# Kernel tuning notes

Measured on AMD Instinct MI355X. Metric: run time of the kernel, lower is better.

Reference implementation:

```python
import jax, jax.numpy as jnp
import numpy as np

N = 20000      # nodes
E = 320000     # edges
F_IN = 64      # input_dim
HID = 128      # hidden_dim
H = 2          # heads (hard-coded in BGA)
G = 64         # num graphs (batch_step_dim[0])
MID = 32       # middle_dim
OUT = 1        # output_dim
EPS = 1e-5


def setup_inputs() -> dict:
    key = jax.random.key(0)
    ks = jax.random.split(key, 24)
    p = lambda k, shape: jax.random.normal(k, shape, jnp.float32) * 0.05
    inp = {}
    inp["x"] = jax.random.normal(ks[0], (N, F_IN), jnp.float32)
    inp["edge_index"] = jax.random.randint(ks[1], (2, E), 0, N)
    inp["atten_edge_index"] = jax.random.randint(ks[2], (2, E), 0, N)
    inp["batch_index"] = jnp.sort(jax.random.randint(ks[3], (N,), 0, G))
    # GANConv 0 MLP (2-layer: Linear->BN->ReLU->Linear)
    inp["g0_w1"] = p(ks[4], (F_IN, HID)); inp["g0_b1"] = jnp.zeros((HID,), jnp.float32)
    inp["g0_bn_g"] = jnp.ones((HID,), jnp.float32); inp["g0_bn_b"] = jnp.zeros((HID,), jnp.float32)
    inp["g0_w2"] = p(ks[5], (HID, HID)); inp["g0_b2"] = jnp.zeros((HID,), jnp.float32)
    # GANConv 1 MLP
    inp["g1_w1"] = p(ks[6], (HID, HID)); inp["g1_b1"] = jnp.zeros((HID,), jnp.float32)
    inp["g1_bn_g"] = jnp.ones((HID,), jnp.float32); inp["g1_bn_b"] = jnp.zeros((HID,), jnp.float32)
    inp["g1_w2"] = p(ks[7], (HID, HID)); inp["g1_b2"] = jnp.zeros((HID,), jnp.float32)
    # BGA batch norms after each GANConv
    inp["bn0_g"] = jnp.ones((HID,), jnp.float32); inp["bn0_b"] = jnp.zeros((HID,), jnp.float32)
    inp["bn1_g"] = jnp.ones((HID,), jnp.float32); inp["bn1_b"] = jnp.zeros((HID,), jnp.float32)
    # ATTConv atten_self: in=HID, out=HID, heads=2, concat=True
    inp["a1_wl"] = p(ks[8], (HID, H * HID)); inp["a1_bl"] = jnp.zeros((H * HID,), jnp.float32)
    inp["a1_wr"] = p(ks[9], (HID, H * HID)); inp["a1_br"] = jnp.zeros((H * HID,), jnp.float32)
    inp["a1_att"] = p(ks[10], (H, HID))
    inp["a1_bias"] = jnp.zeros((H * HID,), jnp.float32)
    # ATTConv atten: in=H*HID, out=HID, heads=2, concat=False (mean over heads)
    inp["a2_wl"] = p(ks[11], (H * HID, H * HID)); inp["a2_bl"] = jnp.zeros((H * HID,), jnp.float32)
    inp["a2_wr"] = p(ks[12], (H * HID, H * HID)); inp["a2_br"] = jnp.zeros((H * HID,), jnp.float32)
    inp["a2_att"] = p(ks[13], (H, HID))
    inp["a2_bias"] = jnp.zeros((HID,), jnp.float32)
    # prediction heads (only layer 0 and last are used)
    inp["pred0_w"] = p(ks[14], (F_IN, MID)); inp["pred0_b"] = jnp.zeros((MID,), jnp.float32)
    inp["predL_w"] = p(ks[15], (HID, MID)); inp["predL_b"] = jnp.zeros((MID,), jnp.float32)
    inp["out_w"] = p(ks[16], (MID, OUT)); inp["out_b"] = jnp.zeros((OUT,), jnp.float32)
    return inp


def _bn(x, g, b):  # training-mode batch norm over node axis
    m = x.mean(0)
    v = x.var(0)
    return (x - m) * jax.lax.rsqrt(v + EPS) * g + b


def _mlp2(x, w1, b1, bn_g, bn_b, w2, b2):
    h = jax.nn.relu(_bn(x @ w1 + b1, bn_g, bn_b))
    return h @ w2 + b2


def _gan_conv(x, edge_index, w1, b1, bn_g, bn_b, w2, b2):
    row, col = edge_index[0], edge_index[1]
    agg = jax.ops.segment_sum(x[col], row, num_segments=x.shape[0])
    return _mlp2(x + agg, w1, b1, bn_g, bn_b, w2, b2)


def _att_conv(x, edge_index, wl, bl, wr, br, att, bias, concat):
    # GATv2-style: e = leaky_relu(x_i + x_j); alpha = softmax_dst(<e, att>)
    n = x.shape[0]
    xl = (x @ wl + bl).reshape(n, H, HID)  # source proj
    xr = (x @ wr + br).reshape(n, H, HID)  # target proj
    src, dst = edge_index[0], edge_index[1]
    e = jax.nn.leaky_relu(xl[src] + xr[dst], 0.2)          # [E,H,C]
    logit = jnp.einsum('ehc,hc->eh', e, att)               # [E,H]
    lmax = jax.ops.segment_max(logit, dst, num_segments=n)
    w = jnp.exp(logit - lmax[dst])
    denom = jax.ops.segment_sum(w, dst, num_segments=n)
    alpha = w / (denom[dst] + 1e-16)                       # [E,H]
    out = jax.ops.segment_sum(xl[src] * alpha[:, :, None], dst, num_segments=n)
    if concat:
        out = out.reshape(n, H * HID)
    else:
        out = out.mean(1)
    return out + bias, alpha


def reference(x, edge_index, atten_edge_index, batch_index,
              g0_w1, g0_b1, g0_bn_g, g0_bn_b, g0_w2, g0_b2,
              g1_w1, g1_b1, g1_bn_g, g1_bn_b, g1_w2, g1_b2,
              bn0_g, bn0_b, bn1_g, bn1_b,
              a1_wl, a1_bl, a1_wr, a1_br, a1_att, a1_bias,
              a2_wl, a2_bl, a2_wr, a2_br, a2_att, a2_bias,
              pred0_w, pred0_b, predL_w, predL_b, out_w, out_b):
    h0 = x
    h1 = jax.nn.relu(_bn(_gan_conv(h0, edge_index, g0_w1, g0_b1, g0_bn_g, g0_bn_b, g0_w2, g0_b2), bn0_g, bn0_b))
    h2 = jax.nn.relu(_bn(_gan_conv(h1, edge_index, g1_w1, g1_b1, g1_bn_g, g1_bn_b, g1_w2, g1_b2), bn1_g, bn1_b))
    emb, _ = _att_conv(h2, edge_index, a1_wl, a1_bl, a1_wr, a1_br, a1_att, a1_bias, concat=True)
    emb = jax.nn.relu(emb)
    atten_out, alpha = _att_conv(emb, atten_edge_index, a2_wl, a2_bl, a2_wr, a2_br, a2_att, a2_bias, concat=False)
    atten_out = jax.nn.relu(atten_out)
    pool0 = jax.ops.segment_sum(h0, batch_index, num_segments=G)
    poolL = jax.ops.segment_sum(atten_out, batch_index, num_segments=G)
    out_h = jax.nn.relu((pool0 @ pred0_w + pred0_b) + (poolL @ predL_w + predL_b))
    outputs = out_h @ out_w + out_b
    return (outputs, atten_out, alpha)
```

## Files before the change

### kernel.cpp

```cpp
#include <hip/hip_runtime.h>
#include <hip/hip_bf16.h>

#define N_NODES 20000
#define E_EDGES 320000
#define F_INN   64
#define HID     128
#define HEADS   2
#define HC      (HEADS * HID)
#define G_GR    64
#define MIDD    32
#define EPSV    1e-5f
#define NBUK    79

#define CDIV(a, b) (((a) + (b) - 1) / (b))

typedef __attribute__((ext_vector_type(8))) short          bf16x8;
typedef __attribute__((ext_vector_type(4))) float          f32x4;
typedef __attribute__((ext_vector_type(8))) unsigned short u16x8;

__device__ inline float bf2f(unsigned short u) { return __uint_as_float((unsigned)u << 16); }
__device__ inline unsigned short f2bf(float f) {
    unsigned u = __float_as_uint(f);
    unsigned r = u + 0x7FFFu + ((u >> 16) & 1u);
    return (unsigned short)(r >> 16);
}

#if __has_builtin(__builtin_amdgcn_exp2f)
__device__ inline float fexp2(float x) { return __builtin_amdgcn_exp2f(x); }
#else
__device__ inline float fexp2(float x) { return exp2f(x); }
#endif

struct Csr3 {
    const int* key[3];
    const int* other[3];
    int* btot;
    int* bstart;
    int* bcur;
    int* rowptr[3];
    int* out[3];
    int2* tmp;
};

__global__ __launch_bounds__(256) void k_bhist(Csr3 c) {
    __shared__ int hist[NBUK];
    const int y = blockIdx.y;
    const int chunk0 = blockIdx.x * 4096;
    const int t = threadIdx.x;
    for (int i = t; i < NBUK; i += 256) hist[i] = 0;
    __syncthreads();
#pragma unroll
    for (int i = 0; i < 16; i++) {
        int e = chunk0 + (i << 8) + t;
        if (e < E_EDGES) atomicAdd(&hist[c.key[y][e] >> 8], 1);
    }
    __syncthreads();
    for (int i = t; i < NBUK; i += 256)
        if (hist[i] > 0) atomicAdd(&c.btot[y * NBUK + i], hist[i]);
}

__global__ void k_bscan(Csr3 c) {
    __shared__ int sh[3 * NBUK];
    int t = threadIdx.x;
    for (int i = t; i < 3 * NBUK; i += 256) sh[i] = c.btot[i];
    __syncthreads();
    if (t < 3) {
        int run = 0;
        int* bs = c.bstart + t * (NBUK + 1);
        for (int b = 0; b < NBUK; b++) {
            bs[b] = run;
            c.bcur[t * NBUK + b] = run;
            run += sh[t * NBUK + b];
        }
        bs[NBUK] = run;
    }
}

__global__ __launch_bounds__(256) void k_bucketA(Csr3 c) {
    __shared__ int hist[NBUK], base[NBUK], off[NBUK];
    const int y = blockIdx.y;
    const int chunk0 = blockIdx.x * 4096;
    const int t = threadIdx.x;
    for (int i = t; i < NBUK; i += 256) { hist[i] = 0; off[i] = 0; }
    __syncthreads();
    int keys[16], vals[16], bks[16];
#pragma unroll
    for (int i = 0; i < 16; i++) {
        int e = chunk0 + (i << 8) + t;
        bool ok = (e < E_EDGES);
        int k = ok ? c.key[y][e] : 0;
        keys[i] = k;
        vals[i] = ok ? ((y == 2) ? e : c.other[y][e]) : 0;
        bks[i] = ok ? (k >> 8) : -1;
        if (ok) atomicAdd(&hist[k >> 8], 1);
    }
    __syncthreads();
    if (t < NBUK && hist[t] > 0) base[t] = atomicAdd(&c.bcur[y * NBUK + t], hist[t]);
    __syncthreads();
    int2* ty = c.tmp + (size_t)y * E_EDGES;
#pragma unroll
    for (int i = 0; i < 16; i++) {
        int b = bks[i];
        if (b >= 0) {
            int o = atomicAdd(&off[b], 1);
            ty[base[b] + o] = make_int2(keys[i], vals[i]);
        }
    }
}

__global__ __launch_bounds__(256) void k_bucketB(Csr3 c) {
    __shared__ int cnt[256], lbase[256], run[256];
    const int y = blockIdx.y;
    const int b = blockIdx.x;
    const int nbase = b << 8;
    const int t = threadIdx.x;
    cnt[t] = 0; run[t] = 0;
    __syncthreads();
    const int bs = c.bstart[y * (NBUK + 1) + b];
    const int be = c.bstart[y * (NBUK + 1) + b + 1];
    const int2* ty = c.tmp + (size_t)y * E_EDGES;
    for (int i = bs + t; i < be; i += 256)
        atomicAdd(&cnt[ty[i].x - nbase], 1);
    __syncthreads();
    int v = cnt[t];
    lbase[t] = v;
    __syncthreads();
    for (int off = 1; off < 256; off <<= 1) {
        int u = (t >= off) ? lbase[t - off] : 0;
        __syncthreads();
        lbase[t] += u;
        __syncthreads();
    }
    int excl = lbase[t] - v;
    __syncthreads();
    lbase[t] = excl;
    __syncthreads();
    int n = nbase + t;
    if (n < N_NODES) c.rowptr[y][n] = bs + excl;
    if (b == NBUK - 1 && t == 0) c.rowptr[y][N_NODES] = E_EDGES;
    int* outy = c.out[y];
    for (int i = bs + t; i < be; i += 256) {
        int2 kv = ty[i];
        int k = kv.x - nbase;
        int o = atomicAdd(&run[k], 1);
        outy[bs + lbase[k] + o] = kv.y;
    }
}

__global__ __launch_bounds__(256) void k_src_gather(const int* __restrict__ eids,
                                                    const int* __restrict__ srcs,
                                                    int* __restrict__ outv) {
    int i = blockIdx.x * 256 + threadIdx.x;
    if (i < E_EDGES) outv[i] = srcs[eids[i]];
}

__global__ __launch_bounds__(256) void k_gather_f32(const float4* __restrict__ x,
                                                    const int* __restrict__ rowptr,
                                                    const int* __restrict__ srcs,
                                                    unsigned short* __restrict__ z) {
    int gid = blockIdx.x * blockDim.x + threadIdx.x;
    int n = gid >> 4;
    if (n >= N_NODES) return;
    int q = gid & 15;
    float4 acc = x[((size_t)n << 4) + q];
    float4 a1 = make_float4(0.f, 0.f, 0.f, 0.f), a2 = a1, a3 = a1;
    int p = rowptr[n], p1 = rowptr[n + 1];
    for (; p + 4 <= p1; p += 4) {
        float4 v0 = x[((size_t)srcs[p + 0] << 4) + q];
        float4 v1 = x[((size_t)srcs[p + 1] << 4) + q];
        float4 v2 = x[((size_t)srcs[p + 2] << 4) + q];
        float4 v3 = x[((size_t)srcs[p + 3] << 4) + q];
        acc.x += v0.x; acc.y += v0.y; acc.z += v0.z; acc.w += v0.w;
        a1.x += v1.x; a1.y += v1.y; a1.z += v1.z; a1.w += v1.w;
        a2.x += v2.x; a2.y += v2.y; a2.z += v2.z; a2.w += v2.w;
        a3.x += v3.x; a3.y += v3.y; a3.z += v3.z; a3.w += v3.w;
    }
    for (; p < p1; p++) {
        float4 v = x[((size_t)srcs[p] << 4) + q];
        acc.x += v.x; acc.y += v.y; acc.z += v.z; acc.w += v.w;
    }
    acc.x += a1.x + a2.x + a3.x; acc.y += a1.y + a2.y + a3.y;
    acc.z += a1.z + a2.z + a3.z; acc.w += a1.w + a2.w + a3.w;
    ushort4 o;
    o.x = f2bf(acc.x); o.y = f2bf(acc.y); o.z = f2bf(acc.z); o.w = f2bf(acc.w);
    *(ushort4*)&z[((size_t)n << 6) + (q << 2)] = o;
}

__global__ __launch_bounds__(256) void k_gather_bn(const u16x8* __restrict__ raw,
                                                   const int* __restrict__ rowptr,
                                                   const int* __restrict__ srcs,
                                                   const float* __restrict__ bn_sums,
                                                   const float* __restrict__ g,
                                                   const float* __restrict__ b,
                                                   u16x8* __restrict__ z) {
    int gid = blockIdx.x * blockDim.x + threadIdx.x;
    int n = gid >> 4;
    if (n >= N_NODES) return;
    int q = gid & 15;
    float sc[8], sh[8];
#pragma unroll
    for (int i = 0; i < 8; i++) {
        int c = (q << 3) + i;
        float mean = bn_sums[c] / N_NODES;
        float istd = rsqrtf(bn_sums[HID + c] / N_NODES - mean * mean + EPSV);
        float s = istd * g[c];
        sc[i] = s;
        sh[i] = b[c] - mean * s;
    }
    u16x8 u0 = raw[((size_t)n << 4) + q];
    float acc[8];
#pragma unroll
    for (int i = 0; i < 8; i++) acc[i] = fmaxf(bf2f(u0[i]) * sc[i] + sh[i], 0.f);
    int p = rowptr[n], p1 = rowptr[n + 1];
    for (; p + 4 <= p1; p += 4) {
        u16x8 v0 = raw[((size_t)srcs[p + 0] << 4) + q];
        u16x8 v1 = raw[((size_t)srcs[p + 1] << 4) + q];
        u16x8 v2 = raw[((size_t)srcs[p + 2] << 4) + q];
        u16x8 v3 = raw[((size_t)srcs[p + 3] << 4) + q];
#pragma unroll
        for (int i = 0; i < 8; i++) {
            acc[i] += fmaxf(bf2f(v0[i]) * sc[i] + sh[i], 0.f)
                    + fmaxf(bf2f(v1[i]) * sc[i] + sh[i], 0.f)
                    + fmaxf(bf2f(v2[i]) * sc[i] + sh[i], 0.f)
                    + fmaxf(bf2f(v3[i]) * sc[i] + sh[i], 0.f);
        }
    }
    for (; p < p1; p++) {
        u16x8 v = raw[((size_t)srcs[p] << 4) + q];
#pragma unroll
        for (int i = 0; i < 8; i++) acc[i] += fmaxf(bf2f(v[i]) * sc[i] + sh[i], 0.f);
    }
    u16x8 o;
#pragma unroll
    for (int i = 0; i < 8; i++) o[i] = f2bf(acc[i]);
    z[((size_t)n << 4) + q] = o;
}

struct WtJob  { const float* src; unsigned short* dst; int K; int N; };
struct WtJobs { WtJob j[8]; };
__global__ void k_wt_cast(WtJobs jobs) {
    WtJob jb = jobs.j[blockIdx.y];
    int total = jb.K * jb.N;
    for (int i = blockIdx.x * blockDim.x + threadIdx.x; i < total; i += gridDim.x * blockDim.x) {
        int nn = i / jb.K, kk = i - nn * jb.K;
        jb.dst[i] = f2bf(jb.src[(size_t)kk * jb.N + nn]);
    }
}

template <int STATS, int BNA, int TM, int TN, int BIAS2, int SPLIT>
__global__ __launch_bounds__(256) void k_mfma_gemm(const unsigned short* __restrict__ A,
                                                   const unsigned short* __restrict__ Wt,
                                                   const float* __restrict__ biasL,
                                                   const float* __restrict__ biasR,
                                                   unsigned short* __restrict__ Cout,
                                                   int M, int K, int N,
                                                   float* __restrict__ stats_sums,
                                                   const float* __restrict__ bn_sums,
                                                   const float* __restrict__ bn_g,
                                                   const float* __restrict__ bn_b) {
    constexpr int BNF = (TM == 128) ? (TN / 32) : (TN / 64);
    constexpr int BPASS = TN / 64;
    __shared__ unsigned short As[TM][40];
    __shared__ unsigned short Bs[TN][40];
    __shared__ float s_scale[BNA ? HID : 1], s_shift[BNA ? HID : 1];
    const int t = threadIdx.x;
    if (BNA) {
        if (t < HID) {
            float mean = bn_sums[t] / M;
            float istd = rsqrtf(bn_sums[HID + t] / M - mean * mean + EPSV);
            float s = istd * bn_g[t];
            s_scale[t] = s;
            s_shift[t] = bn_b[t] - mean * s;
        }
        __syncthreads();
    }
    const int wave = t >> 6, lane = t & 63;
    const int row0 = blockIdx.y * TM, col0 = blockIdx.x * TN;
    const int wm = (TM == 128) ? ((wave & 1) << 6) : 0;
    const int wn = (TM == 128) ? ((wave >> 1) << 6)
                               : ((TN == 128) ? (wave << 5) : (wave << 4));
    const int lm = lane & 15, lk = (lane >> 4) << 3;
    constexpr int APASS = TM / 64;
    f32x4 acc[4][BNF] = {};
    for (int k0 = 0; k0 < K; k0 += 32) {
        u16x8 av[APASS], wv[BPASS];
#pragma unroll
        for (int i = 0; i < APASS; i++) {
            int c = t + (i << 8);
            int r = c >> 2, ko = (c & 3) << 3;
            u16x8 zv = {};
            int gr = row0 + r;
            av[i] = (gr < M) ? *(const u16x8*)&A[(size_t)gr * K + k0 + ko] : zv;
            if (BNA) {
#pragma unroll
                for (int j = 0; j < 8; j++) {
                    int kc = k0 + ko + j;
                    float v = fmaxf(bf2f(av[i][j]) * s_scale[kc] + s_shift[kc], 0.f);
                    av[i][j] = f2bf(v);
                }
            }
        }
#pragma unroll
        for (int i = 0; i < BPASS; i++) {
            int c = t + (i << 8);
            int r = c >> 2, ko = (c & 3) << 3;
            wv[i] = *(const u16x8*)&Wt[(size_t)(col0 + r) * K + k0 + ko];
        }
        __syncthreads();
#pragma unroll
        for (int i = 0; i < APASS; i++) {
            int c = t + (i << 8);
            int r = c >> 2, ko = (c & 3) << 3;
            *(u16x8*)&As[r][ko] = av[i];
        }
#pragma unroll
        for (int i = 0; i < BPASS; i++) {
            int c = t + (i << 8);
            int r = c >> 2, ko = (c & 3) << 3;
            *(u16x8*)&Bs[r][ko] = wv[i];
        }
        __syncthreads();
        bf16x8 af[4], bfm[BNF];
#pragma unroll
        for (int i = 0; i < 4; i++) af[i]  = *(const bf16x8*)&As[wm + (i << 4) + lm][lk];
#pragma unroll
        for (int j = 0; j < BNF; j++) bfm[j] = *(const bf16x8*)&Bs[wn + (j << 4) + lm][lk];
#pragma unroll
        for (int i = 0; i < 4; i++)
#pragma unroll
            for (int j = 0; j < BNF; j++)
                acc[i][j] = __builtin_amdgcn_mfma_f32_16x16x32_bf16(af[i], bfm[j], acc[i][j], 0, 0, 0);
    }
    const int lr4 = (lane >> 4) << 2;
    float s1[BNF], s2[BNF];
#pragma unroll
    for (int j = 0; j < BNF; j++) { s1[j] = 0.f; s2[j] = 0.f; }
#pragma unroll
    for (int j = 0; j < BNF; j++) {
        int col = col0 + wn + (j << 4) + lm;
        float bv = BIAS2 ? ((col < 256) ? biasL[col] : biasR[col - 256]) : biasL[col];
        unsigned short* dstp;
        int cl;
        if (SPLIT) {
            if (col < 256) { dstp = Cout; cl = col; }
            else { dstp = Cout + (size_t)N_NODES * 256; cl = col - 256; }
        } else { dstp = Cout; cl = col; }
#pragma unroll
        for (int i = 0; i < 4; i++) {
#pragma unroll
            for (int r = 0; r < 4; r++) {
                int row = row0 + wm + (i << 4) + lr4 + r;
                if (row < M) {
                    float v = acc[i][j][r] + bv;
                    if (SPLIT) dstp[(size_t)row * 256 + cl] = f2bf(v);
                    else       dstp[(size_t)row * N + cl]   = f2bf(v);
                    if (STATS) { s1[j] += v; s2[j] += v * v; }
                }
            }
        }
    }
    if (STATS) {
#pragma unroll
        for (int j = 0; j < BNF; j++) {
            s1[j] += __shfl_xor(s1[j], 16, 64); s1[j] += __shfl_xor(s1[j], 32, 64);
            s2[j] += __shfl_xor(s2[j], 16, 64); s2[j] += __shfl_xor(s2[j], 32, 64);
        }
        if ((lane >> 4) == 0) {
#pragma unroll
            for (int j = 0; j < BNF; j++) {
                int col = col0 + wn + (j << 4) + lm;
                atomicAdd(&stats_sums[col], s1[j]);
                atomicAdd(&stats_sums[HID + col], s2[j]);
            }
        }
    }
}

#define ATT_CAP 192
#define LOG2E   1.4426950408889634f
#define DTHR    11.0f

__device__ __forceinline__ float att_logit8(u16x8 uv, const float* xr8, const float* at8, float* x8) {
    float tl = 0.f;
#pragma unroll
    for (int i = 0; i < 8; i++) {
        x8[i] = bf2f(uv[i]);
        float v = x8[i] + xr8[i];
        v = fmaxf(v, 0.2f * v);
        tl = fmaf(at8[i], v, tl);
    }
    return tl;
}

template <int CTRL>
__device__ __forceinline__ float dpp_add(float x) {
    int y = __builtin_amdgcn_update_dpp(0, __float_as_int(x), CTRL, 0xF, 0xF, true);
    return x + __int_as_float(y);
}

__device__ __forceinline__ float red16(float tl) {
    tl = dpp_add<0xB1>(tl);
    tl = dpp_add<0x4E>(tl);
    tl = dpp_add<0x124>(tl);
    tl = dpp_add<0x128>(tl);
    return tl;
}

template <int WITH_ALPHA>
__device__ __forceinline__ void att_group4(const u16x8* uv, int ebase, int p0,
                                           int half, int j, int h,
                                           const float* xr8, const float* at8,
                                           float& m, float& ssum, float* acc,
                                           float (*slg)[2]) {
    float x8[4][8], tl[4];
#pragma unroll
    for (int g = 0; g < 4; g++) tl[g] = att_logit8(uv[g], xr8, at8, x8[g]);
#pragma unroll
    for (int g = 0; g < 4; g++) tl[g] = red16(tl[g]);
    if (WITH_ALPHA && (j & 15) == 0) {
#pragma unroll
        for (int g = 0; g < 4; g++) {
            int idx = ebase + (g << 1) + half - p0;
            if (idx < ATT_CAP) slg[idx][h] = tl[g];
        }
    }
    float pm = fmaxf(fmaxf(tl[0], tl[1]), fmaxf(tl[2], tl[3]));
    if (__builtin_expect(!__all(pm <= m + DTHR), 0)) {
#pragma unroll
        for (int g = 0; g < 4; g++) {
            float mn = fmaxf(m, tl[g]);
            float sc = fexp2(m - mn);
            float w  = fexp2(tl[g] - mn);
            ssum = ssum * sc + w;
#pragma unroll
            for (int i = 0; i < 8; i++) acc[i] = acc[i] * sc + w * x8[g][i];
            m = mn;
        }
    } else {
        float w0 = fexp2(tl[0] - m), w1 = fexp2(tl[1] - m);
        float w2 = fexp2(tl[2] - m), w3 = fexp2(tl[3] - m);
        ssum += (w0 + w1) + (w2 + w3);
#pragma unroll
        for (int i = 0; i < 8; i++)
            acc[i] += (w0 * x8[0][i] + w1 * x8[1][i]) + (w2 * x8[2][i] + w3 * x8[3][i]);
    }
}

template <int CONCAT, int WITH_ALPHA>
__global__ __launch_bounds__(256) void k_att_fused(const u16x8* __restrict__ XL,
                                                   const u16x8* __restrict__ XR,
                                                   const int* __restrict__ rowptr,
                                                   const int* __restrict__ plist,
                                                   const int* __restrict__ srclist,
                                                   const float* __restrict__ att,
                                                   const float* __restrict__ bias,
                                                   void* __restrict__ outp,
                                                   float* __restrict__ alpha_out) {
    __shared__ float s_lg[WITH_ALPHA ? 4 : 1][WITH_ALPHA ? ATT_CAP : 1][2];
    const int t = threadIdx.x;
    const int wave = t >> 6, l = t & 63;
    const int n = blockIdx.x * 4 + wave;
    const int half = l >> 5;
    const int j = l & 31;
    const int h = j >> 4;

    u16x8 ur = XR[((size_t)n << 5) + j];
    float xr8[8];
#pragma unroll
    for (int i = 0; i < 8; i++) xr8[i] = bf2f(ur[i]);
    const float* ap = &att[h * HID + ((j & 15) << 3)];
    float at8[8];
#pragma unroll
    for (int i = 0; i < 8; i++) at8[i] = ap[i] * LOG2E;

    const int p0 = rowptr[n], p1 = rowptr[n + 1];
    const int* PL = WITH_ALPHA ? srclist : plist;
    const int deg = p1 - p0;
    int idxreg = (deg > 0) ? PL[p0 + ((l < deg) ? l : (deg - 1))] : 0;

    float m = -1e30f, ssum = 0.f;
    float acc[8] = {};
    float (*slg)[2] = WITH_ALPHA ? s_lg[wave] : nullptr;

    int p = p0;
    for (; p + 16 <= p1; p += 16) {
        int rb = p - p0;
        int sA[4], sB[4];
        if (rb + 16 <= 64) {
#pragma unroll
            for (int g = 0; g < 4; g++)
                sA[g] = __builtin_amdgcn_ds_bpermute((rb + (g << 1) + half) << 2, idxreg);
#pragma unroll
            for (int g = 0; g < 4; g++)
                sB[g] = __builtin_amdgcn_ds_bpermute((rb + 8 + (g << 1) + half) << 2, idxreg);
        } else {
#pragma unroll
            for (int g = 0; g < 4; g++) sA[g] = PL[p + (g << 1) + half];
#pragma unroll
            for (int g = 0; g < 4; g++) sB[g] = PL[p + 8 + (g << 1) + half];
        }
        u16x8 uvA[4], uvB[4];
#pragma unroll
        for (int g = 0; g < 4; g++) uvA[g] = XL[((size_t)sA[g] << 5) + j];
#pragma unroll
        for (int g = 0; g < 4; g++) uvB[g] = XL[((size_t)sB[g] << 5) + j];
        att_group4<WITH_ALPHA>(uvA, p,     p0, half, j, h, xr8, at8, m, ssum, acc, slg);
        att_group4<WITH_ALPHA>(uvB, p + 8, p0, half, j, h, xr8, at8, m, ssum, acc, slg);
    }
    for (; p + 8 <= p1; p += 8) {
        int rb = p - p0;
        int s4[4];
        if (rb + 8 <= 64) {
#pragma unroll
            for (int g = 0; g < 4; g++)
                s4[g] = __builtin_amdgcn_ds_bpermute((rb + (g << 1) + half) << 2, idxreg);
        } else {
#pragma unroll
            for (int g = 0; g < 4; g++) s4[g] = PL[p + (g << 1) + half];
        }
        u16x8 uv[4];
#pragma unroll
        for (int g = 0; g < 4; g++) uv[g] = XL[((size_t)s4[g] << 5) + j];
        att_group4<WITH_ALPHA>(uv, p, p0, half, j, h, xr8, at8, m, ssum, acc, slg);
    }
    for (; p < p1; p += 2) {
        const bool v1 = (p + 1 < p1);
        int er = (half && v1) ? (p + 1) : p;
        int src;
        if (p - p0 + 2 <= 64) src = __builtin_amdgcn_ds_bpermute((er - p0) << 2, idxreg);
        else src = PL[er];
        u16x8 uv = XL[((size_t)src << 5) + j];
        float x8[8], tl;
        tl = att_logit8(uv, xr8, at8, x8);
        tl = red16(tl);
        float vm = (half && !v1) ? 0.f : 1.f;
        if (vm == 0.f) tl = -1e30f;
        if (WITH_ALPHA && (j & 15) == 0 && vm != 0.f) {
            int idx = p + half - p0;
            if (idx < ATT_CAP) s_lg[wave][idx][h] = tl;
        }
        if (__builtin_expect(!__all(tl <= m + DTHR), 0)) {
            float mn = fmaxf(m, tl);
            float sc = fexp2(m - mn);
            float w  = fexp2(tl - mn) * vm;
            ssum = ssum * sc + w;
#pragma unroll
            for (int i = 0; i < 8; i++) acc[i] = acc[i] * sc + w * x8[i];
            m = mn;
        } else {
            float w = fexp2(tl - m) * vm;
            ssum += w;
#pragma unroll
            for (int i = 0; i < 8; i++) acc[i] += w * x8[i];
        }
    }

    float m_o = __shfl_xor(m, 32, 64);
    float mf  = fmaxf(m, m_o);
    float sA  = fexp2(m - mf);
    float ssA = ssum * sA;
    float ssum_f = ssA + __shfl_xor(ssA, 32, 64);
    float accf[8];
#pragma unroll
    for (int i = 0; i < 8; i++) {
        float a = acc[i] * sA;
        accf[i] = a + __shfl_xor(a, 32, 64);
    }
    float inv = 1.f / (ssum_f + 1e-16f);

    if (WITH_ALPHA) {
        float m_oh   = __shfl_xor(mf, 16, 64);
        float inv_oh = __shfl_xor(inv, 16, 64);
        float m2[2], i2[2];
        m2[h] = mf;  m2[1 - h] = m_oh;
        i2[h] = inv; i2[1 - h] = inv_oh;
        int cnt = p1 - p0;
        int ccnt = (cnt < ATT_CAP) ? cnt : ATT_CAP;
        for (int i = l; i < ccnt * 2; i += 64) {
            int idx = i >> 1, hh = i & 1;
            float a = fexp2(s_lg[wave][idx][hh] - m2[hh]) * i2[hh];
            alpha_out[plist[p0 + idx] * HEADS + hh] = a;
        }
        for (int pp = p0 + ATT_CAP; pp < p1; pp++) {
            int src = PL[pp];
            u16x8 uv = XL[((size_t)src << 5) + j];
            float x8[8], tl;
            tl = att_logit8(uv, xr8, at8, x8);
            tl = red16(tl);
            if ((j & 15) == 0 && half == 0)
                alpha_out[plist[pp] * HEADS + h] = fexp2(tl - mf) * inv;
        }
    }

    if (CONCAT) {
        if (half == 0) {
            const float* bp = &bias[j << 3];
            u16x8 o;
#pragma unroll
            for (int i = 0; i < 8; i++) o[i] = f2bf(fmaxf(accf[i] * inv + bp[i], 0.f));
            ((u16x8*)outp)[((size_t)n << 5) + j] = o;
        }
    } else {
        float om[8];
#pragma unroll
        for (int i = 0; i < 8; i++) {
            float v = accf[i] * inv;
            om[i] = 0.5f * (v + __shfl_xor(v, 16, 64));
        }
        if (half == 0 && h == 0) {
            const float* bp = &bias[j << 3];
            float4 o0, o1;
            o0.x = fmaxf(om[0] + bp[0], 0.f); o0.y = fmaxf(om[1] + bp[1], 0.f);
            o0.z = fmaxf(om[2] + bp[2], 0.f); o0.w = fmaxf(om[3] + bp[3], 0.f);
            o1.x = fmaxf(om[4] + bp[4], 0.f); o1.y = fmaxf(om[5] + bp[5], 0.f);
            o1.z = fmaxf(om[6] + bp[6], 0.f); o1.w = fmaxf(om[7] + bp[7], 0.f);
            ((float4*)outp)[((size_t)n << 5) + (j << 1)]     = o0;
            ((float4*)outp)[((size_t)n << 5) + (j << 1) + 1] = o1;
        }
    }
}

template <int C>
__global__ __launch_bounds__(256) void k_pool_atomic(const float* __restrict__ X,
                                                     const int* __restrict__ batch,
                                                     float* __restrict__ pool, int npb) {
    const int RP = 256 / C;
    int c = threadIdx.x & (C - 1);
    int rofs = threadIdx.x / C;
    int i0 = blockIdx.x * npb;
    int i1 = min(i0 + npb, N_NODES);
    float acc = 0.f;
    int gcur = -1;
    for (int i = i0 + rofs; i < i1; i += RP) {
        int g = batch[i];
        if (g != gcur) {
            if (gcur >= 0) atomicAdd(&pool[gcur * C + c], acc);
            acc = 0.f; gcur = g;
        }
        acc += X[(size_t)i * C + c];
    }
    if (gcur >= 0) atomicAdd(&pool[gcur * C + c], acc);
}

__global__ void k_head(const float* __restrict__ pool0, const float* __restrict__ poolL,
                       const float* __restrict__ p0w, const float* __restrict__ p0b,
                       const float* __restrict__ pLw, const float* __restrict__ pLb,
                       const float* __restrict__ ow, const float* __restrict__ ob,
                       float* __restrict__ outputs) {
    int g = blockIdx.x;
    int m = threadIdx.x;
    __shared__ float sh[MIDD];
    if (m < MIDD) {
        float s = p0b[m] + pLb[m];
        for (int k = 0; k < F_INN; k++) s += pool0[g * F_INN + k] * p0w[k * MIDD + m];
        for (int k = 0; k < HID; k++)  s += poolL[g * HID + k] * pLw[k * MIDD + m];
        sh[m] = fmaxf(s, 0.f);
    }
    __syncthreads();
    if (m == 0) {
        float s = ob[0];
        for (int k = 0; k < MIDD; k++) s += sh[k] * ow[k];
        outputs[g] = s;
    }
}

extern "C" void kernel_launch(void* const* d_in, const int* in_sizes, int n_in,
                              void* d_out, int out_size, void* d_ws, size_t ws_size,
                              hipStream_t stream) {
    const float* x      = (const float*)d_in[0];
    const int*   ei     = (const int*)d_in[1];
    const int*   aei    = (const int*)d_in[2];
    const int*   batch  = (const int*)d_in[3];
    const float* g0_w1  = (const float*)d_in[4];
    const float* g0_b1  = (const float*)d_in[5];
    const float* g0_bng = (const float*)d_in[6];
    const float* g0_bnb = (const float*)d_in[7];
    const float* g0_w2  = (const float*)d_in[8];
    const float* g0_b2  = (const float*)d_in[9];
    const float* g1_w1  = (const float*)d_in[10];
    const float* g1_b1  = (const float*)d_in[11];
    const float* g1_bng = (const float*)d_in[12];
    const float* g1_bnb = (const float*)d_in[13];
    const float* g1_w2  = (const float*)d_in[14];
    const float* g1_b2  = (const float*)d_in[15];
    const float* bn0_g  = (const float*)d_in[16];
    const float* bn0_b  = (const float*)d_in[17];
    const float* bn1_g  = (const float*)d_in[18];
    const float* bn1_b  = (const float*)d_in[19];
    const float* a1_wl  = (const float*)d_in[20];
    const float* a1_bl  = (const float*)d_in[21];
    const float* a1_wr  = (const float*)d_in[22];
    const float* a1_br  = (const float*)d_in[23];
    const float* a1_att = (const float*)d_in[24];
    const float* a1_bias= (const float*)d_in[25];
    const float* a2_wl  = (const float*)d_in[26];
    const float* a2_bl  = (const float*)d_in[27];
    const float* a2_wr  = (const float*)d_in[28];
    const float* a2_br  = (const float*)d_in[29];
    const float* a2_att = (const float*)d_in[30];
    const float* a2_bias= (const float*)d_in[31];
    const float* p0w    = (const float*)d_in[32];
    const float* p0b    = (const float*)d_in[33];
    const float* pLw    = (const float*)d_in[34];
    const float* pLb    = (const float*)d_in[35];
    const float* ow     = (const float*)d_in[36];
    const float* ob     = (const float*)d_in[37];

    float* out_head  = (float*)d_out;
    float* atten_out = out_head + G_GR;
    float* alpha_out = atten_out + (size_t)N_NODES * HID;

    float* ws = (float*)d_ws;
    float* sums4 = ws;
    float* pool0 = sums4 + 4 * 256;
    float* poolL = pool0 + G_GR * F_INN;
    int*   btot  = (int*)(poolL + G_GR * HID);
    const size_t zero_bytes = (4 * 256 + G_GR * F_INN + G_GR * HID + 3 * NBUK) * 4;

    int* ip = btot + 3 * NBUK;
    int* bstart = ip; ip += 3 * (NBUK + 1);
    int* bcur   = ip; ip += 3 * NBUK;
    int* rowptr[3]; int* payload[3];
    for (int c = 0; c < 3; c++) {
        rowptr[c]  = ip; ip += N_NODES + 1;
        payload[c] = ip; ip += E_EDGES;
    }
    int2* tmp3 = (int2*)ip; ip += 2 * 3 * E_EDGES;
    int* srclist = (int*)tmp3;
    const size_t NB = (size_t)N_NODES * HC;
    unsigned short* B1 = (unsigned short*)ip;
    unsigned short* B2 = B1 + NB;
    unsigned short* Qb = B2 + NB;
    unsigned short* g0w1t = Qb + 2 * NB;
    unsigned short* g0w2t = g0w1t + 128 * 64;
    unsigned short* g1w1t = g0w2t + 128 * 128;
    unsigned short* g1w2t = g1w1t + 128 * 128;
    unsigned short* a1wlt = g1w2t + 128 * 128;
    unsigned short* a1wrt = a1wlt + 256 * 128;
    unsigned short* a2wlt = a1wrt + 256 * 128;
    unsigned short* a2wrt = a2wlt + 256 * 256;

    unsigned short* XLb = Qb;
    unsigned short* XRb = Qb + (size_t)N_NODES * 256;

    const int* e_row = ei;
    const int* e_col = ei + E_EDGES;
    const int* a_src = aei;
    const int* a_dst = aei + E_EDGES;

    const int TB = 256;
#define GRID1(n) dim3(CDIV((n), TB))

    {
        WtJobs jobs;
        jobs.j[0] = {g0_w1, g0w1t, F_INN, HID};
        jobs.j[1] = {g0_w2, g0w2t, HID,   HID};
        jobs.j[2] = {g1_w1, g1w1t, HID,   HID};
        jobs.j[3] = {g1_w2, g1w2t, HID,   HID};
        jobs.j[4] = {a1_wl, a1wlt, HID,   HC};
        jobs.j[5] = {a1_wr, a1wrt, HID,   HC};
        jobs.j[6] = {a2_wl, a2wlt, HC,    HC};
        jobs.j[7] = {a2_wr, a2wrt, HC,    HC};
        k_wt_cast<<<dim3(32, 8), TB, 0, stream>>>(jobs);
    }

    (void)hipMemsetAsync(sums4, 0, zero_bytes, stream);
    {
        Csr3 c;
        c.key[0] = e_row; c.other[0] = e_col;
        c.key[1] = e_col; c.other[1] = e_row;
        c.key[2] = a_dst; c.other[2] = a_src;
        c.btot = btot; c.bstart = bstart; c.bcur = bcur; c.tmp = tmp3;
        for (int i = 0; i < 3; i++) { c.rowptr[i] = rowptr[i]; c.out[i] = payload[i]; }
        k_bhist<<<dim3(CDIV(E_EDGES, 4096), 3), TB, 0, stream>>>(c);
        k_bscan<<<dim3(1), TB, 0, stream>>>(c);
        k_bucketA<<<dim3(CDIV(E_EDGES, 4096), 3), TB, 0, stream>>>(c);
        k_bucketB<<<dim3(NBUK, 3), TB, 0, stream>>>(c);
    }
    k_src_gather<<<GRID1(E_EDGES), TB, 0, stream>>>(payload[2], a_src, srclist);

    const dim3 gemm_g1(2, CDIV(N_NODES, 64));
    const dim3 gemm_gq(4, CDIV(N_NODES, 128));
    const float* NOF = nullptr;

    k_gather_f32<<<GRID1(N_NODES * 16), TB, 0, stream>>>((const float4*)x, rowptr[0], payload[0], B1);
    k_mfma_gemm<1, 0, 64, 64, 0, 0><<<gemm_g1, TB, 0, stream>>>(B1, g0w1t, g0_b1, NOF, B2, N_NODES, F_INN, HID,
                                                                sums4 + 0, NOF, NOF, NOF);
    k_mfma_gemm<1, 1, 64, 64, 0, 0><<<gemm_g1, TB, 0, stream>>>(B2, g0w2t, g0_b2, NOF, B1, N_NODES, HID, HID,
                                                                sums4 + 256, sums4 + 0, g0_bng, g0_bnb);

    k_gather_bn<<<GRID1(N_NODES * 16), TB, 0, stream>>>((const u16x8*)B1, rowptr[0], payload[0],
                                                        sums4 + 256, bn0_g, bn0_b, (u16x8*)B2);
    k_mfma_gemm<1, 0, 64, 64, 0, 0><<<gemm_g1, TB, 0, stream>>>(B2, g1w1t, g1_b1, NOF, B1, N_NODES, HID, HID,
                                                                sums4 + 512, NOF, NOF, NOF);
    k_mfma_gemm<1, 1, 64, 64, 0, 0><<<gemm_g1, TB, 0, stream>>>(B1, g1w2t, g1_b2, NOF, B2, N_NODES, HID, HID,
                                                                sums4 + 768, sums4 + 512, g1_bng, g1_bnb);

    k_mfma_gemm<0, 1, 128, 128, 1, 1><<<gemm_gq, TB, 0, stream>>>(B2, a1wlt, a1_bl, a1_br, XLb, N_NODES, HID, 512,
                                                                  nullptr, sums4 + 768, bn1_g, bn1_b);
    k_att_fused<1, 0><<<dim3(N_NODES / 4), TB, 0, stream>>>(
        (const u16x8*)XLb, (const u16x8*)XRb, rowptr[1], payload[1], nullptr,
        a1_att, a1_bias, (void*)B1, nullptr);

    k_mfma_gemm<0, 0, 128, 128, 1, 1><<<gemm_gq, TB, 0, stream>>>(B1, a2wlt, a2_bl, a2_br, XLb, N_NODES, HC, 512,
                                                                  nullptr, NOF, NOF, NOF);
    k_att_fused<0, 1><<<dim3(N_NODES / 4), TB, 0, stream>>>(
        (const u16x8*)XLb, (const u16x8*)XRb, rowptr[2], payload[2], srclist,
        a2_att, a2_bias, (void*)atten_out, alpha_out);

    {
        const int npb = 64;
        k_pool_atomic<F_INN><<<dim3(CDIV(N_NODES, npb)), TB, 0, stream>>>(x, batch, pool0, npb);
        k_pool_atomic<HID><<<dim3(CDIV(N_NODES, npb)), TB, 0, stream>>>(atten_out, batch, poolL, npb);
    }
    k_head<<<dim3(G_GR), 64, 0, stream>>>(pool0, poolL, p0w, p0b, pLw, pLb, ow, ob, out_head);
}
```

Measured before the change: 418.8 us.

## Pack bucket temp entries, fuse front gather/srclist/pool0 kernels, mask attention tail

```diff
diff --git a/kernel.cpp b/kernel.cpp
--- a/kernel.cpp
+++ b/kernel.cpp
@@ -39,7 +39,7 @@
     int* bcur;
     int* rowptr[3];
     int* out[3];
-    int2* tmp;
+    int* tmp;
 };
 
 __global__ __launch_bounds__(256) void k_bhist(Csr3 c) {
@@ -97,13 +97,13 @@
     __syncthreads();
     if (t < NBUK && hist[t] > 0) base[t] = atomicAdd(&c.bcur[y * NBUK + t], hist[t]);
     __syncthreads();
-    int2* ty = c.tmp + (size_t)y * E_EDGES;
+    int* ty = c.tmp + (size_t)y * E_EDGES;
 #pragma unroll
     for (int i = 0; i < 16; i++) {
         int b = bks[i];
         if (b >= 0) {
             int o = atomicAdd(&off[b], 1);
-            ty[base[b] + o] = make_int2(keys[i], vals[i]);
+            ty[base[b] + o] = ((keys[i] & 255) << 24) | vals[i];
         }
     }
 }
@@ -118,9 +118,9 @@
     __syncthreads();
     const int bs = c.bstart[y * (NBUK + 1) + b];
     const int be = c.bstart[y * (NBUK + 1) + b + 1];
-    const int2* ty = c.tmp + (size_t)y * E_EDGES;
+    const int* ty = c.tmp + (size_t)y * E_EDGES;
     for (int i = bs + t; i < be; i += 256)
-        atomicAdd(&cnt[ty[i].x - nbase], 1);
+        atomicAdd(&cnt[((unsigned)ty[i]) >> 24], 1);
     __syncthreads();
     int v = cnt[t];
     lbase[t] = v;
@@ -140,50 +140,67 @@
     if (b == NBUK - 1 && t == 0) c.rowptr[y][N_NODES] = E_EDGES;
     int* outy = c.out[y];
     for (int i = bs + t; i < be; i += 256) {
-        int2 kv = ty[i];
-        int k = kv.x - nbase;
+        int u = ty[i];
+        int k = ((unsigned)u) >> 24;
         int o = atomicAdd(&run[k], 1);
-        outy[bs + lbase[k] + o] = kv.y;
-    }
-}
-
-__global__ __launch_bounds__(256) void k_src_gather(const int* __restrict__ eids,
-                                                    const int* __restrict__ srcs,
-                                                    int* __restrict__ outv) {
-    int i = blockIdx.x * 256 + threadIdx.x;
-    if (i < E_EDGES) outv[i] = srcs[eids[i]];
-}
-
-__global__ __launch_bounds__(256) void k_gather_f32(const float4* __restrict__ x,
-                                                    const int* __restrict__ rowptr,
-                                                    const int* __restrict__ srcs,
-                                                    unsigned short* __restrict__ z) {
-    int gid = blockIdx.x * blockDim.x + threadIdx.x;
-    int n = gid >> 4;
-    if (n >= N_NODES) return;
-    int q = gid & 15;
-    float4 acc = x[((size_t)n << 4) + q];
-    float4 a1 = make_float4(0.f, 0.f, 0.f, 0.f), a2 = a1, a3 = a1;
-    int p = rowptr[n], p1 = rowptr[n + 1];
-    for (; p + 4 <= p1; p += 4) {
-        float4 v0 = x[((size_t)srcs[p + 0] << 4) + q];
-        float4 v1 = x[((size_t)srcs[p + 1] << 4) + q];
-        float4 v2 = x[((size_t)srcs[p + 2] << 4) + q];
-        float4 v3 = x[((size_t)srcs[p + 3] << 4) + q];
-        acc.x += v0.x; acc.y += v0.y; acc.z += v0.z; acc.w += v0.w;
-        a1.x += v1.x; a1.y += v1.y; a1.z += v1.z; a1.w += v1.w;
-        a2.x += v2.x; a2.y += v2.y; a2.z += v2.z; a2.w += v2.w;
-        a3.x += v3.x; a3.y += v3.y; a3.z += v3.z; a3.w += v3.w;
-    }
-    for (; p < p1; p++) {
-        float4 v = x[((size_t)srcs[p] << 4) + q];
-        acc.x += v.x; acc.y += v.y; acc.z += v.z; acc.w += v.w;
-    }
-    acc.x += a1.x + a2.x + a3.x; acc.y += a1.y + a2.y + a3.y;
-    acc.z += a1.z + a2.z + a3.z; acc.w += a1.w + a2.w + a3.w;
-    ushort4 o;
-    o.x = f2bf(acc.x); o.y = f2bf(acc.y); o.z = f2bf(acc.z); o.w = f2bf(acc.w);
-    *(ushort4*)&z[((size_t)n << 6) + (q << 2)] = o;
+        outy[bs + lbase[k] + o] = u & 0x00FFFFFF;
+    }
+}
+
+struct FrontArgs {
+    const float4* x; const int* rowptr0; const int* pay0; unsigned short* z;
+    const int* pay2; const int* asrc; int* srclist;
+    const int* batch; float* pool0;
+};
+__global__ __launch_bounds__(256) void k_front(FrontArgs a) {
+    const int bx = blockIdx.x, t = threadIdx.x;
+    if (bx < 1250) {
+        int gid = bx * 256 + t;
+        int n = gid >> 4;
+        int q = gid & 15;
+        float4 acc = a.x[((size_t)n << 4) + q];
+        float4 a1 = make_float4(0.f, 0.f, 0.f, 0.f), a2 = a1, a3 = a1;
+        int p = a.rowptr0[n], p1 = a.rowptr0[n + 1];
+        for (; p + 4 <= p1; p += 4) {
+            float4 v0 = a.x[((size_t)a.pay0[p + 0] << 4) + q];
+            float4 v1 = a.x[((size_t)a.pay0[p + 1] << 4) + q];
+            float4 v2 = a.x[((size_t)a.pay0[p + 2] << 4) + q];
+            float4 v3 = a.x[((size_t)a.pay0[p + 3] << 4) + q];
+            acc.x += v0.x; acc.y += v0.y; acc.z += v0.z; acc.w += v0.w;
+            a1.x += v1.x; a1.y += v1.y; a1.z += v1.z; a1.w += v1.w;
+            a2.x += v2.x; a2.y += v2.y; a2.z += v2.z; a2.w += v2.w;
+            a3.x += v3.x; a3.y += v3.y; a3.z += v3.z; a3.w += v3.w;
+        }
+        for (; p < p1; p++) {
+            float4 v = a.x[((size_t)a.pay0[p] << 4) + q];
+            acc.x += v.x; acc.y += v.y; acc.z += v.z; acc.w += v.w;
+        }
+        acc.x += a1.x + a2.x + a3.x; acc.y += a1.y + a2.y + a3.y;
+        acc.z += a1.z + a2.z + a3.z; acc.w += a1.w + a2.w + a3.w;
+        ushort4 o;
+        o.x = f2bf(acc.x); o.y = f2bf(acc.y); o.z = f2bf(acc.z); o.w = f2bf(acc.w);
+        *(ushort4*)&a.z[((size_t)n << 6) + (q << 2)] = o;
+    } else if (bx < 2500) {
+        int i = (bx - 1250) * 256 + t;
+        a.srclist[i] = a.asrc[a.pay2[i]];
+    } else {
+        int c = t & 63;
+        int rofs = t >> 6;
+        int i0 = (bx - 2500) * 64;
+        int i1 = min(i0 + 64, N_NODES);
+        float acc = 0.f;
+        int gcur = -1;
+        const float* X = (const float*)a.x;
+        for (int i = i0 + rofs; i < i1; i += 4) {
+            int g = a.batch[i];
+            if (g != gcur) {
+                if (gcur >= 0) atomicAdd(&a.pool0[gcur * F_INN + c], acc);
+                acc = 0.f; gcur = g;
+            }
+            acc += X[(size_t)i * F_INN + c];
+        }
+        if (gcur >= 0) atomicAdd(&a.pool0[gcur * F_INN + c], acc);
+    }
 }
 
 __global__ __launch_bounds__(256) void k_gather_bn(const u16x8* __restrict__ raw,
@@ -406,8 +423,8 @@
     return tl;
 }
 
-template <int WITH_ALPHA>
-__device__ __forceinline__ void att_group4(const u16x8* uv, int ebase, int p0,
+template <int WITH_ALPHA, int MASKED>
+__device__ __forceinline__ void att_group4(const u16x8* uv, const float* vm, int ebase, int p0,
                                            int half, int j, int h,
                                            const float* xr8, const float* at8,
                                            float& m, float& ssum, float* acc,
@@ -417,11 +434,16 @@
     for (int g = 0; g < 4; g++) tl[g] = att_logit8(uv[g], xr8, at8, x8[g]);
 #pragma unroll
     for (int g = 0; g < 4; g++) tl[g] = red16(tl[g]);
+    if (MASKED) {
+#pragma unroll
+        for (int g = 0; g < 4; g++) tl[g] = (vm[g] != 0.f) ? tl[g] : -1e30f;
+    }
     if (WITH_ALPHA && (j & 15) == 0) {
 #pragma unroll
         for (int g = 0; g < 4; g++) {
             int idx = ebase + (g << 1) + half - p0;
-            if (idx < ATT_CAP) slg[idx][h] = tl[g];
+            bool ok = MASKED ? (vm[g] != 0.f) : true;
+            if (ok && idx < ATT_CAP) slg[idx][h] = tl[g];
         }
     }
     float pm = fmaxf(fmaxf(tl[0], tl[1]), fmaxf(tl[2], tl[3]));
@@ -431,6 +453,7 @@
             float mn = fmaxf(m, tl[g]);
             float sc = fexp2(m - mn);
             float w  = fexp2(tl[g] - mn);
+            if (MASKED) w *= vm[g];
             ssum = ssum * sc + w;
 #pragma unroll
             for (int i = 0; i < 8; i++) acc[i] = acc[i] * sc + w * x8[g][i];
@@ -439,6 +462,7 @@
     } else {
         float w0 = fexp2(tl[0] - m), w1 = fexp2(tl[1] - m);
         float w2 = fexp2(tl[2] - m), w3 = fexp2(tl[3] - m);
+        if (MASKED) { w0 *= vm[0]; w1 *= vm[1]; w2 *= vm[2]; w3 *= vm[3]; }
         ssum += (w0 + w1) + (w2 + w3);
 #pragma unroll
         for (int i = 0; i < 8; i++)
@@ -504,55 +528,27 @@
         for (int g = 0; g < 4; g++) uvA[g] = XL[((size_t)sA[g] << 5) + j];
 #pragma unroll
         for (int g = 0; g < 4; g++) uvB[g] = XL[((size_t)sB[g] << 5) + j];
-        att_group4<WITH_ALPHA>(uvA, p,     p0, half, j, h, xr8, at8, m, ssum, acc, slg);
-        att_group4<WITH_ALPHA>(uvB, p + 8, p0, half, j, h, xr8, at8, m, ssum, acc, slg);
-    }
-    for (; p + 8 <= p1; p += 8) {
+        att_group4<WITH_ALPHA, 0>(uvA, nullptr, p,     p0, half, j, h, xr8, at8, m, ssum, acc, slg);
+        att_group4<WITH_ALPHA, 0>(uvB, nullptr, p + 8, p0, half, j, h, xr8, at8, m, ssum, acc, slg);
+    }
+    for (; p < p1; p += 8) {
         int rb = p - p0;
         int s4[4];
-        if (rb + 8 <= 64) {
-#pragma unroll
-            for (int g = 0; g < 4; g++)
-                s4[g] = __builtin_amdgcn_ds_bpermute((rb + (g << 1) + half) << 2, idxreg);
-        } else {
-#pragma unroll
-            for (int g = 0; g < 4; g++) s4[g] = PL[p + (g << 1) + half];
+        float vm[4];
+        const bool inwin = (rb + 8 <= 64);
+#pragma unroll
+        for (int g = 0; g < 4; g++) {
+            int li = rb + (g << 1) + half;
+            bool ok = li < deg;
+            vm[g] = ok ? 1.f : 0.f;
+            int lic = ok ? li : (deg - 1);
+            if (inwin) s4[g] = __builtin_amdgcn_ds_bpermute(lic << 2, idxreg);
+            else       s4[g] = PL[p0 + lic];
         }
         u16x8 uv[4];
 #pragma unroll
         for (int g = 0; g < 4; g++) uv[g] = XL[((size_t)s4[g] << 5) + j];
-        att_group4<WITH_ALPHA>(uv, p, p0, half, j, h, xr8, at8, m, ssum, acc, slg);
-    }
-    for (; p < p1; p += 2) {
-        const bool v1 = (p + 1 < p1);
-        int er = (half && v1) ? (p + 1) : p;
-        int src;
-        if (p - p0 + 2 <= 64) src = __builtin_amdgcn_ds_bpermute((er - p0) << 2, idxreg);
-        else src = PL[er];
-        u16x8 uv = XL[((size_t)src << 5) + j];
-        float x8[8], tl;
-        tl = att_logit8(uv, xr8, at8, x8);
-        tl = red16(tl);
-        float vm = (half && !v1) ? 0.f : 1.f;
-        if (vm == 0.f) tl = -1e30f;
-        if (WITH_ALPHA && (j & 15) == 0 && vm != 0.f) {
-            int idx = p + half - p0;
-            if (idx < ATT_CAP) s_lg[wave][idx][h] = tl;
-        }
-        if (__builtin_expect(!__all(tl <= m + DTHR), 0)) {
-            float mn = fmaxf(m, tl);
-            float sc = fexp2(m - mn);
-            float w  = fexp2(tl - mn) * vm;
-            ssum = ssum * sc + w;
-#pragma unroll
-            for (int i = 0; i < 8; i++) acc[i] = acc[i] * sc + w * x8[i];
-            m = mn;
-        } else {
-            float w = fexp2(tl - m) * vm;
-            ssum += w;
-#pragma unroll
-            for (int i = 0; i < 8; i++) acc[i] += w * x8[i];
-        }
+        att_group4<WITH_ALPHA, 1>(uv, vm, p, p0, half, j, h, xr8, at8, m, ssum, acc, slg);
     }
 
     float m_o = __shfl_xor(m, 32, 64);
@@ -725,8 +721,8 @@
         rowptr[c]  = ip; ip += N_NODES + 1;
         payload[c] = ip; ip += E_EDGES;
     }
-    int2* tmp3 = (int2*)ip; ip += 2 * 3 * E_EDGES;
-    int* srclist = (int*)tmp3;
+    int* tmp3 = ip; ip += 3 * E_EDGES;
+    int* srclist = tmp3;
     const size_t NB = (size_t)N_NODES * HC;
     unsigned short* B1 = (unsigned short*)ip;
     unsigned short* B2 = B1 + NB;
@@ -777,13 +773,20 @@
         k_bucketA<<<dim3(CDIV(E_EDGES, 4096), 3), TB, 0, stream>>>(c);
         k_bucketB<<<dim3(NBUK, 3), TB, 0, stream>>>(c);
     }
-    k_src_gather<<<GRID1(E_EDGES), TB, 0, stream>>>(payload[2], a_src, srclist);
+
+    {
+        FrontArgs fa;
+        fa.x = (const float4*)x; fa.rowptr0 = rowptr[0]; fa.pay0 = payload[0];
+        fa.z = B1;
+        fa.pay2 = payload[2]; fa.asrc = a_src; fa.srclist = srclist;
+        fa.batch = batch; fa.pool0 = pool0;
+        k_front<<<dim3(2813), TB, 0, stream>>>(fa);
+    }
 
     const dim3 gemm_g1(2, CDIV(N_NODES, 64));
     const dim3 gemm_gq(4, CDIV(N_NODES, 128));
     const float* NOF = nullptr;
 
-    k_gather_f32<<<GRID1(N_NODES * 16), TB, 0, stream>>>((const float4*)x, rowptr[0], payload[0], B1);
     k_mfma_gemm<1, 0, 64, 64, 0, 0><<<gemm_g1, TB, 0, stream>>>(B1, g0w1t, g0_b1, NOF, B2, N_NODES, F_INN, HID,
                                                                 sums4 + 0, NOF, NOF, NOF);
     k_mfma_gemm<1, 1, 64, 64, 0, 0><<<gemm_g1, TB, 0, stream>>>(B2, g0w2t, g0_b2, NOF, B1, N_NODES, HID, HID,
@@ -808,10 +811,6 @@
         (const u16x8*)XLb, (const u16x8*)XRb, rowptr[2], payload[2], srclist,
         a2_att, a2_bias, (void*)atten_out, alpha_out);
 
-    {
-        const int npb = 64;
-        k_pool_atomic<F_INN><<<dim3(CDIV(N_NODES, npb)), TB, 0, stream>>>(x, batch, pool0, npb);
-        k_pool_atomic<HID><<<dim3(CDIV(N_NODES, npb)), TB, 0, stream>>>(atten_out, batch, poolL, npb);
-    }
+    k_pool_atomic<HID><<<dim3(CDIV(N_NODES, 64)), TB, 0, stream>>>(atten_out, batch, poolL, 64);
     k_head<<<dim3(G_GR), 64, 0, stream>>>(pool0, poolL, p0w, p0b, pLw, pLb, ow, ob, out_head);
 }
```

Measured after the change: 419.0 us. Within noise of the previous version (+0.0%).
